# Kernel optimization log

Hardware: AMD Instinct MI355X
Metric: run time of the kernel (lower is better)

## Reference

```python
import jax, jax.numpy as jnp
import numpy as np

# Module config (matches init_kwargs)
G, K, S = 64, 3, 2          # base patch size, num scales, scale factor
B, H, W, C = 64, 512, 512, 3
HG, HL = 128, 128
D_IN = K * G * G * C


def setup_inputs() -> dict:
    key = jax.random.key(0)
    kx, kl, k1, k2 = jax.random.split(key, 4)
    x = jax.random.normal(kx, (B, H, W, C), dtype=jnp.float32)
    # glimpse locations in [-1, 1)
    l = jax.random.uniform(kl, (B, 2), minval=-1.0, maxval=1.0, dtype=jnp.float32)
    # fc1: phi (D_IN -> HG); fc2: l (2 -> HL). PyTorch-Linear-like scale.
    W1 = jax.random.normal(k1, (D_IN, HG), dtype=jnp.float32) / np.sqrt(D_IN)
    b1 = jnp.zeros((HG,), dtype=jnp.float32)
    W2 = jax.random.normal(k2, (2, HL), dtype=jnp.float32) / np.sqrt(2.0)
    b2 = jnp.zeros((HL,), dtype=jnp.float32)
    return {"x": x, "l": l, "W1": W1, "b1": b1, "W2": W2, "b2": b2}


def _extract_glimpse(x, l):
    """Retina: k multi-scale patches centered at l, resized to (G,G).
    Returns (B, K, G, G, C)."""
    sizes = [G * S**i for i in range(K)]              # 64, 128, 256
    pad = sizes[-1] // 2 + 1                          # pad once for largest scale
    xp = jnp.pad(x, ((0, 0), (pad, pad), (pad, pad), (0, 0)))
    # denormalize: [-1,1] -> [0,H], truncated to int (torch .long())
    coords = (0.5 * (l + 1.0) * H).astype(jnp.int32)  # (B,2): col0=x, col1=y
    patches = []
    for size in sizes:
        fy = coords[:, 1] - size // 2 + pad
        fx = coords[:, 0] - size // 2 + pad

        def slice_one(img, y0, x0, size=size):
            return jax.lax.dynamic_slice(img, (y0, x0, 0), (size, size, C))

        p = jax.vmap(slice_one)(xp, fy, fx)           # (B, size, size, C)
        f = size // G
        if f > 1:  # downsample by integer factor via average pooling
            p = p.reshape(B, G, f, G, f, C).mean(axis=(2, 4))
        patches.append(p)
    return jnp.stack(patches, axis=1)                 # (B, K, G, G, C)


def reference(x, l, W1, b1, W2, b2):
    phi = _extract_glimpse(x, l).reshape(x.shape[0], -1)   # (B, K*G*G*C)
    phi_out = jax.nn.relu(phi @ W1 + b1)                   # (B, HG)
    l_out = jax.nn.relu(l @ W2 + b2)                       # (B, HL)
    return jax.nn.relu(jnp.concatenate([phi_out, l_out], axis=1))
```

## Files before the change

### kernel.cpp

```cpp
#include <hip/hip_runtime.h>
#include <hip/hip_bf16.h>

#define G_     64
#define NK     3
#define NB     64
#define IH     512
#define IW     512
#define NC     3
#define HG_    128
#define HL_    128
#define D_IN_    (NK * G_ * G_ * NC)
#define D_SCALE  (G_ * G_ * NC)
#define KCH      128
#define NCHUNK   (D_IN_ / KCH)
#define BSPLIT   4
#define NBLK     (NCHUNK * BSPLIT)
#define PSTRIDE  (NB * HG_)

template <int F>
__device__ __forceinline__ void scale_body(
    const float* __restrict__ x, const float* __restrict__ l,
    const float* __restrict__ W1, float* __restrict__ P,
    int roff, int d0, int b0, int chunkGlobal,
    float (&phi_s)[16][KCH], int* cx_s, int* cy_s)
{
    const int tid = threadIdx.x;
    if (tid < 16) {
        float lx = l[(b0 + tid) * 2 + 0];
        float ly = l[(b0 + tid) * 2 + 1];
        cx_s[tid] = (int)((0.5f * (lx + 1.0f)) * 512.0f);
        cy_s[tid] = (int)((0.5f * (ly + 1.0f)) * 512.0f);
    }
    __syncthreads();

    const int dd   = tid & (KCH - 1);
    const int jb0  = (tid >> 7) * 8;
    const int r    = roff + dd;
    const int gy   = r / (G_ * NC);
    const int rem  = r - gy * (G_ * NC);
    const int gx   = rem / NC;
    const int c    = rem - gx * NC;
    constexpr float inv = 1.0f / (float)(F * F);
    constexpr int JU = (F == 4) ? 2 : 8;

#pragma unroll 1
    for (int jo = 0; jo < 8; jo += JU) {
        float sums[JU];
#pragma unroll
        for (int ji = 0; ji < JU; ++ji) {
            const int jb = jb0 + jo + ji;
            const int b  = b0 + jb;
            const int by = cy_s[jb] - 32 * F + gy * F;
            const int bx = cx_s[jb] - 32 * F + gx * F;
            const float* bimg = x + (size_t)b * (IH * IW * NC) + c;
            float s = 0.0f;
#pragma unroll
            for (int dy = 0; dy < F; ++dy) {
                const int y = by + dy;
                const bool yok = (unsigned)y < (unsigned)IH;
#pragma unroll
                for (int dx = 0; dx < F; ++dx) {
                    const int xx = bx + dx;
                    const bool ok = yok && ((unsigned)xx < (unsigned)IW);
                    s += ok ? bimg[(size_t)y * (IW * NC) + xx * NC] : 0.0f;
                }
            }
            sums[ji] = s;
        }
#pragma unroll
        for (int ji = 0; ji < JU; ++ji)
            phi_s[jb0 + jo + ji][dd] = sums[ji] * inv;
    }
    __syncthreads();

    const int h0 = (tid & 31) * 4;
    const int bl = (tid >> 5) * 2;
    float a0[4] = {0, 0, 0, 0}, a1[4] = {0, 0, 0, 0};
    const float* wp = W1 + (size_t)d0 * HG_ + h0;
    const float4* prow0 = (const float4*)phi_s[bl];
    const float4* prow1 = (const float4*)phi_s[bl + 1];

#pragma unroll 2
    for (int t = 0; t < KCH / 4; ++t) {
        float4 p0v = prow0[t];
        float4 p1v = prow1[t];
#pragma unroll
        for (int u = 0; u < 4; ++u) {
            float4 wv = *(const float4*)(wp + (size_t)(4 * t + u) * HG_);
            float p0 = (&p0v.x)[u];
            float p1 = (&p1v.x)[u];
            a0[0] = fmaf(p0, wv.x, a0[0]);
            a0[1] = fmaf(p0, wv.y, a0[1]);
            a0[2] = fmaf(p0, wv.z, a0[2]);
            a0[3] = fmaf(p0, wv.w, a0[3]);
            a1[0] = fmaf(p1, wv.x, a1[0]);
            a1[1] = fmaf(p1, wv.y, a1[1]);
            a1[2] = fmaf(p1, wv.z, a1[2]);
            a1[3] = fmaf(p1, wv.w, a1[3]);
        }
    }
    float* pb = P + (size_t)chunkGlobal * PSTRIDE + (b0 + bl) * HG_ + h0;
    *(float4*)pb            = make_float4(a0[0], a0[1], a0[2], a0[3]);
    *(float4*)(pb + HG_)    = make_float4(a1[0], a1[1], a1[2], a1[3]);
}

__global__ __launch_bounds__(256) void fused(
    const float* __restrict__ x, const float* __restrict__ l,
    const float* __restrict__ W1, float* __restrict__ P)
{
    __shared__ float phi_s[16][KCH];
    __shared__ int cx_s[16], cy_s[16];

    const int chunkGlobal = blockIdx.x >> 2;
    const int b0 = (blockIdx.x & 3) * 16;
    const int d0 = chunkGlobal * KCH;
    const int chunkLocal = chunkGlobal % 96;
    const int roff = chunkLocal * KCH;

    if (chunkGlobal < 96) {
        scale_body<1>(x, l, W1, P, roff, d0, b0, chunkGlobal, phi_s, cx_s, cy_s);
    } else if (chunkGlobal < 192) {
        scale_body<2>(x, l, W1, P, roff, d0, b0, chunkGlobal, phi_s, cx_s, cy_s);
    } else {
        scale_body<4>(x, l, W1, P, roff, d0, b0, chunkGlobal, phi_s, cx_s, cy_s);
    }
}

__global__ __launch_bounds__(256) void reduce_epilogue(
    const float* __restrict__ P,
    const float* __restrict__ l,
    const float* __restrict__ b1,
    const float* __restrict__ W2,
    const float* __restrict__ b2,
    float* __restrict__ out)
{
    __shared__ float red[HG_];
    const int b = blockIdx.x;
    const int t = threadIdx.x;
    const int h = t & (HG_ - 1);
    const int half = t >> 7;

    float s = 0.0f;
    const float* p = P + (size_t)(half * 144) * PSTRIDE + b * HG_ + h;
#pragma unroll 8
    for (int c = 0; c < 144; ++c)
        s += p[(size_t)c * PSTRIDE];

    if (half == 1) red[h] = s;
    __syncthreads();

    if (half == 0) {
        out[b * (HG_ + HL_) + h] = fmaxf(s + red[h] + b1[h], 0.0f);
    } else {
        float l0 = l[b * 2 + 0];
        float l1 = l[b * 2 + 1];
        float v = fmaf(l1, W2[HL_ + h], fmaf(l0, W2[h], b2[h]));
        out[b * (HG_ + HL_) + HG_ + h] = fmaxf(v, 0.0f);
    }
}

extern "C" void kernel_launch(void* const* d_in, const int* in_sizes, int n_in,
                              void* d_out, int out_size, void* d_ws, size_t ws_size,
                              hipStream_t stream) {
    const float* x  = (const float*)d_in[0];
    const float* l  = (const float*)d_in[1];
    const float* W1 = (const float*)d_in[2];
    const float* b1 = (const float*)d_in[3];
    const float* W2 = (const float*)d_in[4];
    const float* b2 = (const float*)d_in[5];
    float* out = (float*)d_out;
    float* P = (float*)d_ws;

    fused<<<NBLK, 256, 0, stream>>>(x, l, W1, P);
    reduce_epilogue<<<NB, 256, 0, stream>>>(P, l, b1, W2, b2, out);
}
```

Measured before the change: 290.3 us.

## Split pooling into row-coalesced pass writing phi, then separate GEMM kernel

The fused gather-plus-GEMM kernel is split in two. A new pool kernel uses one wavefront per (batch, scale, output row) to read contiguous image rows with coalesced loads, staging them in LDS and reducing them into channel sums. It writes the pooled phi matrix to workspace, and a separate GEMM kernel reads it with float4 loads. This replaces the strided per-element gathers of the old kernel, at the cost of an extra launch and a round trip of phi through global memory.

```diff
diff --git a/kernel.cpp b/kernel.cpp
--- a/kernel.cpp
+++ b/kernel.cpp
@@ -18,58 +18,98 @@
 #define PSTRIDE  (NB * HG_)
 
 template <int F>
-__device__ __forceinline__ void scale_body(
+__device__ __forceinline__ void pool_body(
     const float* __restrict__ x, const float* __restrict__ l,
-    const float* __restrict__ W1, float* __restrict__ P,
-    int roff, int d0, int b0, int chunkGlobal,
-    float (&phi_s)[16][KCH], int* cx_s, int* cy_s)
+    float* __restrict__ phi, int k, int gy, int b,
+    float* __restrict__ lds_row, float* __restrict__ lds_out)
 {
+    const int lane = threadIdx.x & 63;
+    const float lx = l[b * 2 + 0];
+    const float ly = l[b * 2 + 1];
+    const int cx = (int)((0.5f * (lx + 1.0f)) * 512.0f);
+    const int cy = (int)((0.5f * (ly + 1.0f)) * 512.0f);
+    const int bx  = cx - 32 * F;
+    const int by0 = cy - 32 * F + gy * F;
+    constexpr float inv = 1.0f / (float)(F * F);
+
+    float a0 = 0.0f, a1 = 0.0f, a2 = 0.0f;
+    const float* xb = x + (size_t)b * (IH * IW * NC);
+
+#pragma unroll
+    for (int dy = 0; dy < F; ++dy) {
+        const int y = by0 + dy;
+        const bool yok = (unsigned)y < (unsigned)IH;
+        const int rowoff = y * (IW * NC) + bx * NC;
+#pragma unroll
+        for (int ch = 0; ch < 3 * F; ++ch) {
+            const int j  = ch * 64 + lane;
+            const int px = bx + j / 3;
+            const bool ok = yok && ((unsigned)px < (unsigned)IW);
+            lds_row[ch * 64 + lane] = ok ? xb[rowoff + j] : 0.0f;
+        }
+        if constexpr (F == 4) {
+            const float4* p = (const float4*)(lds_row + lane * 12);
+            float4 t0 = p[0], t1 = p[1], t2 = p[2];
+            a0 += t0.x + t0.w + t1.z + t2.y;
+            a1 += t0.y + t1.x + t1.w + t2.z;
+            a2 += t0.z + t1.y + t2.x + t2.w;
+        } else if constexpr (F == 2) {
+            const float2* p = (const float2*)(lds_row + lane * 6);
+            float2 t0 = p[0], t1 = p[1], t2 = p[2];
+            a0 += t0.x + t1.y;
+            a1 += t0.y + t2.x;
+            a2 += t1.x + t2.y;
+        } else {
+            a0 += lds_row[lane * 3 + 0];
+            a1 += lds_row[lane * 3 + 1];
+            a2 += lds_row[lane * 3 + 2];
+        }
+    }
+    a0 *= inv; a1 *= inv; a2 *= inv;
+
+    lds_out[lane * 3 + 0] = a0;
+    lds_out[lane * 3 + 1] = a1;
+    lds_out[lane * 3 + 2] = a2;
+    float* op = phi + (size_t)b * D_IN_ + (size_t)((k * 64 + gy) * 64) * 3;
+#pragma unroll
+    for (int ch = 0; ch < 3; ++ch)
+        op[ch * 64 + lane] = lds_out[ch * 64 + lane];
+}
+
+__global__ __launch_bounds__(256) void pool(
+    const float* __restrict__ x, const float* __restrict__ l,
+    float* __restrict__ phi)
+{
+    __shared__ float lds[4][960];
+    const int wv    = threadIdx.x >> 6;
+    const int k     = blockIdx.x >> 10;
+    const int local = blockIdx.x & 1023;
+    const int gy    = local >> 4;
+    const int b     = (local & 15) * 4 + wv;
+    float* lr = lds[wv];
+    float* lo = lds[wv] + 768;
+    if (k == 0)      pool_body<1>(x, l, phi, 0, gy, b, lr, lo);
+    else if (k == 1) pool_body<2>(x, l, phi, 1, gy, b, lr, lo);
+    else             pool_body<4>(x, l, phi, 2, gy, b, lr, lo);
+}
+
+__global__ __launch_bounds__(256) void gemm_p(
+    const float* __restrict__ phi, const float* __restrict__ W1,
+    float* __restrict__ P)
+{
+    __shared__ float phi_s[16][KCH];
     const int tid = threadIdx.x;
-    if (tid < 16) {
-        float lx = l[(b0 + tid) * 2 + 0];
-        float ly = l[(b0 + tid) * 2 + 1];
-        cx_s[tid] = (int)((0.5f * (lx + 1.0f)) * 512.0f);
-        cy_s[tid] = (int)((0.5f * (ly + 1.0f)) * 512.0f);
-    }
-    __syncthreads();
+    const int chunkGlobal = blockIdx.x >> 2;
+    const int b0 = (blockIdx.x & 3) * 16;
+    const int d0 = chunkGlobal * KCH;
 
-    const int dd   = tid & (KCH - 1);
-    const int jb0  = (tid >> 7) * 8;
-    const int r    = roff + dd;
-    const int gy   = r / (G_ * NC);
-    const int rem  = r - gy * (G_ * NC);
-    const int gx   = rem / NC;
-    const int c    = rem - gx * NC;
-    constexpr float inv = 1.0f / (float)(F * F);
-    constexpr int JU = (F == 4) ? 2 : 8;
-
-#pragma unroll 1
-    for (int jo = 0; jo < 8; jo += JU) {
-        float sums[JU];
-#pragma unroll
-        for (int ji = 0; ji < JU; ++ji) {
-            const int jb = jb0 + jo + ji;
-            const int b  = b0 + jb;
-            const int by = cy_s[jb] - 32 * F + gy * F;
-            const int bx = cx_s[jb] - 32 * F + gx * F;
-            const float* bimg = x + (size_t)b * (IH * IW * NC) + c;
-            float s = 0.0f;
-#pragma unroll
-            for (int dy = 0; dy < F; ++dy) {
-                const int y = by + dy;
-                const bool yok = (unsigned)y < (unsigned)IH;
-#pragma unroll
-                for (int dx = 0; dx < F; ++dx) {
-                    const int xx = bx + dx;
-                    const bool ok = yok && ((unsigned)xx < (unsigned)IW);
-                    s += ok ? bimg[(size_t)y * (IW * NC) + xx * NC] : 0.0f;
-                }
-            }
-            sums[ji] = s;
-        }
-#pragma unroll
-        for (int ji = 0; ji < JU; ++ji)
-            phi_s[jb0 + jo + ji][dd] = sums[ji] * inv;
+    {
+        const int r  = tid >> 5;
+        const int c4 = (tid & 31) * 4;
+        float4 v0 = *(const float4*)(phi + (size_t)(b0 + r) * D_IN_ + d0 + c4);
+        float4 v1 = *(const float4*)(phi + (size_t)(b0 + r + 8) * D_IN_ + d0 + c4);
+        *(float4*)&phi_s[r][c4]     = v0;
+        *(float4*)&phi_s[r + 8][c4] = v1;
     }
     __syncthreads();
 
@@ -100,30 +140,8 @@
         }
     }
     float* pb = P + (size_t)chunkGlobal * PSTRIDE + (b0 + bl) * HG_ + h0;
-    *(float4*)pb            = make_float4(a0[0], a0[1], a0[2], a0[3]);
-    *(float4*)(pb + HG_)    = make_float4(a1[0], a1[1], a1[2], a1[3]);
-}
-
-__global__ __launch_bounds__(256) void fused(
-    const float* __restrict__ x, const float* __restrict__ l,
-    const float* __restrict__ W1, float* __restrict__ P)
-{
-    __shared__ float phi_s[16][KCH];
-    __shared__ int cx_s[16], cy_s[16];
-
-    const int chunkGlobal = blockIdx.x >> 2;
-    const int b0 = (blockIdx.x & 3) * 16;
-    const int d0 = chunkGlobal * KCH;
-    const int chunkLocal = chunkGlobal % 96;
-    const int roff = chunkLocal * KCH;
-
-    if (chunkGlobal < 96) {
-        scale_body<1>(x, l, W1, P, roff, d0, b0, chunkGlobal, phi_s, cx_s, cy_s);
-    } else if (chunkGlobal < 192) {
-        scale_body<2>(x, l, W1, P, roff, d0, b0, chunkGlobal, phi_s, cx_s, cy_s);
-    } else {
-        scale_body<4>(x, l, W1, P, roff, d0, b0, chunkGlobal, phi_s, cx_s, cy_s);
-    }
+    *(float4*)pb         = make_float4(a0[0], a0[1], a0[2], a0[3]);
+    *(float4*)(pb + HG_) = make_float4(a1[0], a1[1], a1[2], a1[3]);
 }
 
 __global__ __launch_bounds__(256) void reduce_epilogue(
@@ -169,8 +187,10 @@
     const float* W2 = (const float*)d_in[4];
     const float* b2 = (const float*)d_in[5];
     float* out = (float*)d_out;
-    float* P = (float*)d_ws;
+    float* P   = (float*)d_ws;
+    float* phi = (float*)((char*)d_ws + (16 << 20));
 
-    fused<<<NBLK, 256, 0, stream>>>(x, l, W1, P);
+    pool<<<3072, 256, 0, stream>>>(x, l, phi);
+    gemm_p<<<NBLK, 256, 0, stream>>>(phi, W1, P);
     reduce_epilogue<<<NB, 256, 0, stream>>>(P, l, b1, W2, b2, out);
 }
```

Result: slower. 310.1 us (+6.8%).
